# Optimization experiments

Measured on AMD Instinct MI355X. Metric: run time of the kernel, lower is better.

The kernel has to match this reference:

```python
import jax, jax.numpy as jnp
import numpy as np

D_MODEL = 1024
B, S = 4, 2048


def setup_inputs() -> dict:
    key = jax.random.key(0)
    kx, km, kq, kk, kv, ko = jax.random.split(key, 6)
    x = jax.random.normal(kx, (B, S, D_MODEL), dtype=jnp.float32)
    mask = jax.random.randint(km, (B, S, S), 0, 2).astype(jnp.bool_)
    # flax Dense default kernel init: lecun_normal-ish; plain scaled normal is fine for a reference
    init_scale = 1.0 / np.sqrt(D_MODEL)
    Wq = jax.random.normal(kq, (D_MODEL, D_MODEL), dtype=jnp.float32) * init_scale
    Wk = jax.random.normal(kk, (D_MODEL, D_MODEL), dtype=jnp.float32) * init_scale
    Wv = jax.random.normal(kv, (D_MODEL, D_MODEL), dtype=jnp.float32) * init_scale
    Wo = jax.random.normal(ko, (D_MODEL, D_MODEL), dtype=jnp.float32) * init_scale
    return {"x": x, "mask": mask, "Wq": Wq, "Wk": Wk, "Wv": Wv, "Wo": Wo}


def reference(x, mask, Wq, Wk, Wv, Wo):
    # QKV projections (use_bias=False)
    q = jnp.einsum('bsd,de->bse', x, Wq)
    k = jnp.einsum('bsd,de->bse', x, Wk)
    v = jnp.einsum('bsd,de->bse', x, Wv)
    scale = jnp.sqrt(jnp.asarray(q.shape[-1], x.dtype)).astype(x.dtype)
    # [B, S, S] attention scores
    attn_scores = jnp.einsum('bqd,bkd->bqk', q, k) / scale
    attn_scores = jnp.where(mask, attn_scores, jnp.asarray(-1e10, x.dtype))
    attn_weights = jax.nn.softmax(attn_scores, axis=-1)
    attn_output = jnp.einsum('bqk,bkd->bqd', attn_weights, v)
    return jnp.einsum('bsd,de->bse', attn_output, Wo)
```

## Files before the change

kernel.cpp:

```cpp
#include <hip/hip_runtime.h>


#define DM 1024
#define SQ 2048
#define NB 4
typedef unsigned short U16;
typedef short bhalf8 __attribute__((ext_vector_type(8)));
typedef float f32x4 __attribute__((ext_vector_type(4)));

__device__ inline U16 f2bf(float f) {
  unsigned int u = __float_as_uint(f);
  u += 0x7FFFu + ((u >> 16) & 1u);
  return (U16)(u >> 16);
}
__device__ inline float2 bfp2(unsigned int u) {
  float2 r;
  r.x = __uint_as_float(u << 16);
  r.y = __uint_as_float(u & 0xffff0000u);
  return r;
}
__device__ inline unsigned int packbf(float a, float b) {
  return (unsigned int)f2bf(a) | ((unsigned int)f2bf(b) << 16);
}

__global__ __launch_bounds__(256) void conv_f32_bf16(
    const float* __restrict__ src, U16* __restrict__ dst, float* __restrict__ rs) {
  int idx = blockIdx.x * 256 + threadIdx.x;
  if (idx < NB * SQ) rs[idx] = 0.f;
  int i = idx * 8;
  float4 a = *(const float4*)(src + i);
  float4 b = *(const float4*)(src + i + 4);
  uint4 w;
  w.x = packbf(a.x, a.y); w.y = packbf(a.z, a.w);
  w.z = packbf(b.x, b.y); w.w = packbf(b.z, b.w);
  *(uint4*)(dst + i) = w;
}

__device__ inline void ldcvt16(const float* p, U16* d) {
#pragma unroll
  for (int i = 0; i < 4; ++i) {
    float4 f = *(const float4*)(p + i * 4);
    d[i * 4 + 0] = f2bf(f.x); d[i * 4 + 1] = f2bf(f.y);
    d[i * 4 + 2] = f2bf(f.z); d[i * 4 + 3] = f2bf(f.w);
  }
}
__device__ inline void ldcvt16(const U16* p, U16* d) {
  uint4 a = *(const uint4*)p;
  uint4 b = *(const uint4*)(p + 8);
  *(uint4*)d = a;
  *(uint4*)(d + 8) = b;
}

__global__ __launch_bounds__(256) void transp_w4(
    const float* __restrict__ Wq, const float* __restrict__ Wk,
    const float* __restrict__ Wo, const float* __restrict__ Wv,
    U16* __restrict__ WT, U16* __restrict__ WoT, U16* __restrict__ Wv16) {
  __shared__ U16 tile[64][72];
  const int z = blockIdx.z;
  const int r0 = blockIdx.y * 64, c0 = blockIdx.x * 64;
  const int t = threadIdx.x;
  const int tr = t >> 2, tc = (t & 3) * 16;
  if (z == 3) {
    U16 vals[16];
    ldcvt16(Wv + (size_t)(r0 + tr) * DM + c0 + tc, vals);
    U16* op = Wv16 + (size_t)(r0 + tr) * DM + c0 + tc;
    *(uint4*)op = *(uint4*)&vals[0];
    *(uint4*)(op + 8) = *(uint4*)&vals[8];
    return;
  }
  const float* src = (z == 0) ? Wq : (z == 1) ? Wk : Wo;
  U16* d = (z == 2) ? WoT : WT + (size_t)z * DM * DM;
  ldcvt16(src + (size_t)(r0 + tr) * DM + c0 + tc, &tile[tr][tc]);
  __syncthreads();
  U16 vals[16];
#pragma unroll
  for (int m = 0; m < 16; ++m) vals[m] = tile[tc + m][tr];
  U16* op = d + (size_t)(c0 + tr) * DM + r0 + tc;
  *(uint4*)op = *(uint4*)&vals[0];
  *(uint4*)(op + 8) = *(uint4*)&vals[8];
}

__global__ __launch_bounds__(256) void transp_bf16(
    const U16* __restrict__ src, U16* __restrict__ dst, int R, int C) {
  __shared__ U16 tile[64][72];
  const int z = blockIdx.z;
  src += (size_t)z * R * C;
  dst += (size_t)z * R * C;
  const int r0 = blockIdx.y * 64, c0 = blockIdx.x * 64;
  const int t = threadIdx.x;
  const int tr = t >> 2, tc = (t & 3) * 16;
  ldcvt16(src + (size_t)(r0 + tr) * C + c0 + tc, &tile[tr][tc]);
  __syncthreads();
  U16 vals[16];
#pragma unroll
  for (int m = 0; m < 16; ++m) vals[m] = tile[tc + m][tr];
  U16* op = dst + (size_t)(c0 + tr) * R + r0 + tc;
  *(uint4*)op = *(uint4*)&vals[0];
  *(uint4*)(op + 8) = *(uint4*)&vals[8];
}

template <int EP>
__global__ __launch_bounds__(256) void gemm_mfma(
    const U16* __restrict__ A, const U16* __restrict__ B, void* __restrict__ Cv,
    int M, int N, int K, long long sA, long long sB, long long sC,
    const int* __restrict__ mask, float* __restrict__ rowsum, float scale) {
  __shared__ U16 As[128 * 72];
  __shared__ U16 Bs[128 * 72];
  const int t = threadIdx.x;
  const int lane = t & 63, wave = t >> 6;
  const int wm = wave >> 1, wn = wave & 1;
  const int q = lane >> 4, ln = lane & 15;
  const int z = blockIdx.z;
  const int m0 = blockIdx.y * 128, n0 = blockIdx.x * 128;
  A += (size_t)z * sA;
  B += (size_t)z * sB;

  f32x4 acc[4][4] = {};

  const int srow = t >> 3;
  const int scol = (t & 7) * 8;

  for (int k0 = 0; k0 < K; k0 += 64) {
    const U16* ga = A + (size_t)(m0 + srow) * K + k0 + scol;
    const U16* gb = B + (size_t)(n0 + srow) * K + k0 + scol;
#pragma unroll
    for (int it = 0; it < 4; ++it) {
      uint4 va = *(const uint4*)(ga + (size_t)it * 32 * K);
      uint4 vb = *(const uint4*)(gb + (size_t)it * 32 * K);
      *(uint4*)&As[(it * 32 + srow) * 72 + scol] = va;
      *(uint4*)&Bs[(it * 32 + srow) * 72 + scol] = vb;
    }
    __syncthreads();
#pragma unroll
    for (int kk = 0; kk < 64; kk += 32) {
      bhalf8 af[4], bg[4];
#pragma unroll
      for (int i = 0; i < 4; ++i) {
        af[i] = *(const bhalf8*)&As[(wm * 64 + i * 16 + ln) * 72 + kk + q * 8];
        bg[i] = *(const bhalf8*)&Bs[(wn * 64 + i * 16 + ln) * 72 + kk + q * 8];
      }
#pragma unroll
      for (int i = 0; i < 4; ++i)
#pragma unroll
        for (int j = 0; j < 4; ++j)
          acc[i][j] = __builtin_amdgcn_mfma_f32_16x16x32_bf16(af[i], bg[j], acc[i][j], 0, 0, 0);
    }
    __syncthreads();
  }

#pragma unroll
  for (int i = 0; i < 4; ++i) {
#pragma unroll
    for (int r = 0; r < 4; ++r) {
      const int rr = m0 + wm * 64 + i * 16 + q * 4 + r;
      float linv = 0.f;
      if constexpr (EP == 2) linv = 1.0f / (rowsum[(size_t)z * M + rr] + 1e-30f);
      float psum = 0.f;
#pragma unroll
      for (int j = 0; j < 4; ++j) {
        const int c = n0 + wn * 64 + j * 16 + ln;
        float v = acc[i][j][r];
        if constexpr (EP == 0) {
          ((U16*)Cv)[(size_t)z * sC + (size_t)rr * N + c] = f2bf(v);
        } else if constexpr (EP == 1) {
          int mk = mask[((size_t)z * M + rr) * N + c];
          float p = mk ? __expf(v * scale) : 0.f;
          U16 pb = f2bf(p);
          ((U16*)Cv)[(size_t)z * sC + (size_t)rr * N + c] = pb;
          psum += __uint_as_float((unsigned int)pb << 16);
        } else {
          ((float*)Cv)[(size_t)z * sC + (size_t)rr * N + c] = v * linv;
        }
      }
      if constexpr (EP == 1) {
#pragma unroll
        for (int off = 8; off > 0; off >>= 1) psum += __shfl_xor(psum, off, 64);
        if (ln == 0) atomicAdd(&rowsum[(size_t)z * M + rr], psum);
      }
    }
  }
}

__device__ inline float4 load4(const float* p) { return *(const float4*)p; }
__device__ inline float4 load4(const U16* p) {
  uint2 w = *(const uint2*)p;
  float2 f0 = bfp2(w.x), f1 = bfp2(w.y);
  return make_float4(f0.x, f0.y, f1.x, f1.y);
}
__device__ inline void store4(float* p, float a, float b, float c, float d) {
  *(float4*)p = make_float4(a, b, c, d);
}
__device__ inline void store4(U16* p, float a, float b, float c, float d) {
  uint2 w;
  w.x = packbf(a, b);
  w.y = packbf(c, d);
  *(uint2*)p = w;
}
template <typename TA, typename TB, typename TC>
__global__ __launch_bounds__(256) void gemm_t(
    const TA* __restrict__ A, const TB* __restrict__ B,
    TC* __restrict__ C, int M, int N, int K) {
  __shared__ float As[16][64];
  __shared__ float Bs[16][64];
  const int t = threadIdx.x;
  const int tx = t & 15, ty = t >> 4;
  const int m0 = blockIdx.y * 64;
  const int n0 = blockIdx.x * 64;
  const int arow = t >> 2, akq = (t & 3) * 4;
  const int brow = t >> 4, bcg = (t & 15) * 4;
  float acc[4][4] = {};
  for (int k0 = 0; k0 < K; k0 += 16) {
    {
      float4 f = load4(A + (size_t)(m0 + arow) * K + k0 + akq);
      As[akq + 0][arow] = f.x; As[akq + 1][arow] = f.y;
      As[akq + 2][arow] = f.z; As[akq + 3][arow] = f.w;
    }
    {
      float4 f = load4(B + (size_t)(k0 + brow) * N + n0 + bcg);
      *(float4*)&Bs[brow][bcg] = f;
    }
    __syncthreads();
#pragma unroll
    for (int kk = 0; kk < 16; ++kk) {
      float4 a = *(const float4*)&As[kk][ty * 4];
      float4 b = *(const float4*)&Bs[kk][tx * 4];
      float av[4] = {a.x, a.y, a.z, a.w};
      float bv[4] = {b.x, b.y, b.z, b.w};
#pragma unroll
      for (int i = 0; i < 4; ++i)
#pragma unroll
        for (int j = 0; j < 4; ++j) acc[i][j] += av[i] * bv[j];
    }
    __syncthreads();
  }
#pragma unroll
  for (int i = 0; i < 4; ++i)
    store4(&C[(size_t)(m0 + ty * 4 + i) * N + n0 + tx * 4],
           acc[i][0], acc[i][1], acc[i][2], acc[i][3]);
}
__global__ __launch_bounds__(256) void flash_wave(
    const U16* __restrict__ Q, const U16* __restrict__ Kd,
    const U16* __restrict__ V, const int* __restrict__ mask,
    U16* __restrict__ O) {
  __shared__ float q_s[4][DM];
  const int t = threadIdx.x;
  const int w = t >> 6;
  const int lane = t & 63;
  const int row = blockIdx.x * 4 + w;
  const int b = row >> 11;
  const size_t bo = (size_t)b * SQ * DM;
  const size_t mrow0 = (size_t)row * SQ;
  {
    const U16* qp = Q + (size_t)row * DM + lane * 16;
    uint4 w0 = *(const uint4*)qp;
    uint4 w1 = *(const uint4*)(qp + 8);
    float* dst = &q_s[w][lane * 16];
    float2 f;
    f = bfp2(w0.x); dst[0] = f.x;  dst[1] = f.y;
    f = bfp2(w0.y); dst[2] = f.x;  dst[3] = f.y;
    f = bfp2(w0.z); dst[4] = f.x;  dst[5] = f.y;
    f = bfp2(w0.w); dst[6] = f.x;  dst[7] = f.y;
    f = bfp2(w1.x); dst[8] = f.x;  dst[9] = f.y;
    f = bfp2(w1.y); dst[10] = f.x; dst[11] = f.y;
    f = bfp2(w1.z); dst[12] = f.x; dst[13] = f.y;
    f = bfp2(w1.w); dst[14] = f.x; dst[15] = f.y;
  }
  __syncthreads();
  float m = -3.0e38f, l = 0.f;
  float o[16] = {};
  const int dbase = lane * 16;
  const float* qrow = q_s[w];
  for (int j0 = 0; j0 < SQ; j0 += 64) {
    float s;
    {
      const U16* kp = Kd + bo + (size_t)(j0 + lane) * DM;
      float acc = 0.f;
      for (int d = 0; d < DM; d += 8) {
        uint4 kw = *(const uint4*)(kp + d);
        float2 a0 = bfp2(kw.x), a1 = bfp2(kw.y), a2 = bfp2(kw.z), a3 = bfp2(kw.w);
        acc += qrow[d] * a0.x + qrow[d + 1] * a0.y + qrow[d + 2] * a1.x +
               qrow[d + 3] * a1.y + qrow[d + 4] * a2.x + qrow[d + 5] * a2.y +
               qrow[d + 6] * a3.x + qrow[d + 7] * a3.y;
      }
      s = acc * 0.03125f;
      if (mask[mrow0 + j0 + lane] == 0) s = -1e10f;
    }
    float ms = s;
#pragma unroll
    for (int off = 32; off > 0; off >>= 1) ms = fmaxf(ms, __shfl_xor(ms, off, 64));
    float mn = fmaxf(m, ms);
    float alpha = __expf(m - mn);
    float p = __expf(s - mn);
    float ps = p;
#pragma unroll
    for (int off = 32; off > 0; off >>= 1) ps += __shfl_xor(ps, off, 64);
    l = l * alpha + ps;
    m = mn;
#pragma unroll
    for (int k = 0; k < 16; ++k) o[k] *= alpha;
    const U16* vp = V + bo + (size_t)j0 * DM + dbase;
    for (int j = 0; j < 64; ++j) {
      float pj = __shfl(p, j, 64);
      uint4 v0 = *(const uint4*)(vp + (size_t)j * DM);
      uint4 v1 = *(const uint4*)(vp + (size_t)j * DM + 8);
      float2 f0 = bfp2(v0.x), f1 = bfp2(v0.y), f2 = bfp2(v0.z), f3 = bfp2(v0.w);
      float2 g0 = bfp2(v1.x), g1 = bfp2(v1.y), g2 = bfp2(v1.z), g3 = bfp2(v1.w);
      o[0] += pj * f0.x;  o[1] += pj * f0.y;  o[2] += pj * f1.x;  o[3] += pj * f1.y;
      o[4] += pj * f2.x;  o[5] += pj * f2.y;  o[6] += pj * f3.x;  o[7] += pj * f3.y;
      o[8] += pj * g0.x;  o[9] += pj * g0.y;  o[10] += pj * g1.x; o[11] += pj * g1.y;
      o[12] += pj * g2.x; o[13] += pj * g2.y; o[14] += pj * g3.x; o[15] += pj * g3.y;
    }
  }
  float linv = (l > 0.f) ? (1.0f / l) : 0.f;
  U16* op = O + (size_t)row * DM + dbase;
  uint4 r0, r1;
  r0.x = packbf(o[0] * linv, o[1] * linv);
  r0.y = packbf(o[2] * linv, o[3] * linv);
  r0.z = packbf(o[4] * linv, o[5] * linv);
  r0.w = packbf(o[6] * linv, o[7] * linv);
  r1.x = packbf(o[8] * linv, o[9] * linv);
  r1.y = packbf(o[10] * linv, o[11] * linv);
  r1.z = packbf(o[12] * linv, o[13] * linv);
  r1.w = packbf(o[14] * linv, o[15] * linv);
  *(uint4*)op = r0;
  *(uint4*)(op + 8) = r1;
}

extern "C" void kernel_launch(void* const* d_in, const int* in_sizes, int n_in,
                              void* d_out, int out_size, void* d_ws, size_t ws_size,
                              hipStream_t stream) {
  const float* x  = (const float*)d_in[0];
  const int* mask = (const int*)d_in[1];
  const float* Wq = (const float*)d_in[2];
  const float* Wk = (const float*)d_in[3];
  const float* Wv = (const float*)d_in[4];
  const float* Wo = (const float*)d_in[5];
  float* out = (float*)d_out;

  const size_t MB = 1u << 20;
  const size_t E = (size_t)NB * SQ * DM;
  const size_t WE = (size_t)DM * DM;

  if (ws_size >= 121 * MB) {
    char* ws = (char*)d_ws;
    U16* WT   = (U16*)ws;
    U16* WoT  = (U16*)(ws + 6 * MB);
    U16* x16  = (U16*)(ws + 8 * MB);
    U16* Q16  = (U16*)(ws + 24 * MB);
    U16* K16  = (U16*)(ws + 40 * MB);
    U16* U16b = (U16*)(ws + 56 * MB);
    U16* Wv16 = (U16*)(ws + 72 * MB);
    U16* UT16 = (U16*)(ws + 72 * MB);
    U16* P16  = (U16*)(ws + 88 * MB);
    float* rs = (float*)(ws + 120 * MB);

    conv_f32_bf16<<<dim3(E / (256 * 8)), 256, 0, stream>>>(x, x16, rs);
    transp_w4<<<dim3(16, 16, 4), 256, 0, stream>>>(Wq, Wk, Wo, Wv, WT, WoT, Wv16);

    gemm_mfma<0><<<dim3(DM / 128, DM / 128, 1), 256, 0, stream>>>(
        WoT, Wv16, WT + 2 * WE, DM, DM, DM, 0, 0, 0, nullptr, nullptr, 0.f);

    gemm_mfma<0><<<dim3(DM / 128, (NB * SQ) / 128, 3), 256, 0, stream>>>(
        x16, WT, Q16, NB * SQ, DM, DM,
        0, (long long)WE, (long long)E, nullptr, nullptr, 0.f);

    transp_bf16<<<dim3(DM / 64, SQ / 64, NB), 256, 0, stream>>>(U16b, UT16, SQ, DM);

    gemm_mfma<1><<<dim3(SQ / 128, SQ / 128, NB), 256, 0, stream>>>(
        Q16, K16, P16, SQ, SQ, DM,
        (long long)SQ * DM, (long long)SQ * DM, (long long)SQ * SQ,
        mask, rs, 0.03125f);

    gemm_mfma<2><<<dim3(DM / 128, SQ / 128, NB), 256, 0, stream>>>(
        P16, UT16, out, SQ, DM, SQ,
        (long long)SQ * SQ, (long long)DM * SQ, (long long)SQ * DM,
        nullptr, rs, 0.f);
  } else {
    U16* Kw = (U16*)d_ws;
    U16* Vw = Kw + E;
    U16* Qw = Vw + E;
    U16* Ow = Qw;
    dim3 blk(256);
    dim3 gg(DM / 64, (NB * SQ) / 64);
    gemm_t<float, float, U16><<<gg, blk, 0, stream>>>(x, Wk, Kw, NB * SQ, DM, DM);
    gemm_t<float, float, U16><<<gg, blk, 0, stream>>>(x, Wv, Vw, NB * SQ, DM, DM);
    gemm_t<float, float, U16><<<gg, blk, 0, stream>>>(x, Wq, Qw, NB * SQ, DM, DM);
    flash_wave<<<dim3((NB * SQ) / 4), blk, 0, stream>>>(Qw, Kw, Vw, mask, Ow);
    gemm_t<U16, float, float><<<gg, blk, 0, stream>>>(Ow, Wo, out, NB * SQ, DM, DM);
  }
}
```

Measured before the change: 358.2 us.

## Add double-buffered direct-to-LDS GEMM with larger tiles for main matmuls

Introduces a new 512-thread GEMM kernel that loads A/B tiles straight into LDS with global_load_lds_dwordx4 and double-buffers them, so the next tile's load overlaps the current tile's MFMA work. Block tiles grow to 256x128 or 256x256, which raises data reuse per block. The QKV projection, the masked-score GEMM and the PV GEMM all switch to it. In exchange, LDS use is larger and occupancy lower, and the unpadded 64-wide LDS rows may cause bank conflicts on the fragment reads. The grid for the score GEMM also shrinks, which can hurt load balance.

After: 348.1 us. 1.03x faster.

```diff
diff --git a/kernel.cpp b/kernel.cpp
--- a/kernel.cpp
+++ b/kernel.cpp
@@ -21,6 +21,16 @@
 }
 __device__ inline unsigned int packbf(float a, float b) {
   return (unsigned int)f2bf(a) | ((unsigned int)f2bf(b) << 16);
+}
+
+__device__ __forceinline__ void gload16(const U16* g, const U16* l) {
+  unsigned int m0v =
+      (unsigned int)__builtin_amdgcn_readfirstlane((int)(unsigned long long)l);
+  asm volatile("s_mov_b32 m0, %0\n\t"
+               "global_load_lds_dwordx4 %1, off"
+               :
+               : "s"(m0v), "v"(g)
+               : "memory");
 }
 
 __global__ __launch_bounds__(256) void conv_f32_bf16(
@@ -153,6 +163,112 @@
 #pragma unroll
     for (int r = 0; r < 4; ++r) {
       const int rr = m0 + wm * 64 + i * 16 + q * 4 + r;
+      float linv = 0.f;
+      if constexpr (EP == 2) linv = 1.0f / (rowsum[(size_t)z * M + rr] + 1e-30f);
+      float psum = 0.f;
+#pragma unroll
+      for (int j = 0; j < 4; ++j) {
+        const int c = n0 + wn * 64 + j * 16 + ln;
+        float v = acc[i][j][r];
+        if constexpr (EP == 0) {
+          ((U16*)Cv)[(size_t)z * sC + (size_t)rr * N + c] = f2bf(v);
+        } else if constexpr (EP == 1) {
+          int mk = mask[((size_t)z * M + rr) * N + c];
+          float p = mk ? __expf(v * scale) : 0.f;
+          U16 pb = f2bf(p);
+          ((U16*)Cv)[(size_t)z * sC + (size_t)rr * N + c] = pb;
+          psum += __uint_as_float((unsigned int)pb << 16);
+        } else {
+          ((float*)Cv)[(size_t)z * sC + (size_t)rr * N + c] = v * linv;
+        }
+      }
+      if constexpr (EP == 1) {
+#pragma unroll
+        for (int off = 8; off > 0; off >>= 1) psum += __shfl_xor(psum, off, 64);
+        if (ln == 0) atomicAdd(&rowsum[(size_t)z * M + rr], psum);
+      }
+    }
+  }
+}
+
+template <int EP, int FM>
+__global__ __launch_bounds__(512) void gemm2(
+    const U16* __restrict__ A, const U16* __restrict__ B, void* __restrict__ Cv,
+    int M, int N, int K, long long sA, long long sB, long long sC,
+    const int* __restrict__ mask, float* __restrict__ rowsum, float scale) {
+  constexpr int WN = (FM == 4) ? 2 : 4;
+  constexpr int BN = WN * 64;
+  __shared__ __attribute__((aligned(16))) U16 As[2][256 * 64];
+  __shared__ __attribute__((aligned(16))) U16 Bs[2][BN * 64];
+  const int t = threadIdx.x;
+  const int lane = t & 63, wave = t >> 6;
+  const int wm = wave / WN, wn = wave % WN;
+  const int q = lane >> 4, ln = lane & 15;
+  const int z = blockIdx.z;
+  const int m0 = blockIdx.y * 256, n0 = blockIdx.x * BN;
+  const U16* Ab = A + (size_t)z * sA + (size_t)m0 * K;
+  const U16* Bb = B + (size_t)z * sB + (size_t)n0 * K;
+  const U16* gA = Ab + (size_t)(wave * 8 + (lane >> 3)) * K + (lane & 7) * 8;
+  const U16* gB = Bb + (size_t)(wave * 8 + (lane >> 3)) * K + (lane & 7) * 8;
+  const U16* lA = &As[0][wave * 8 * 64];
+  const U16* lB = &Bs[0][wave * 8 * 64];
+
+  f32x4 acc[FM][4] = {};
+  const int NT = K >> 6;
+
+#define STAGE2(bufi, koff)                                                   \
+  {                                                                          \
+    _Pragma("unroll") for (int c = 0; c < 4; ++c)                            \
+        gload16(gA + (size_t)(c * 64) * K + (koff),                          \
+                lA + (bufi) * (256 * 64) + c * (64 * 64));                   \
+    _Pragma("unroll") for (int c = 0; c < BN / 64; ++c)                      \
+        gload16(gB + (size_t)(c * 64) * K + (koff),                          \
+                lB + (bufi) * (BN * 64) + c * (64 * 64));                    \
+  }
+
+#define COMPUTE2(bufi)                                                       \
+  {                                                                          \
+    _Pragma("unroll") for (int kk = 0; kk < 64; kk += 32) {                  \
+      bhalf8 af[FM], bg[4];                                                  \
+      _Pragma("unroll") for (int i = 0; i < FM; ++i)                         \
+          af[i] = *(const bhalf8*)&As[bufi][(wm * (FM * 16) + i * 16 + ln) * 64 + kk + q * 8]; \
+      _Pragma("unroll") for (int j = 0; j < 4; ++j)                          \
+          bg[j] = *(const bhalf8*)&Bs[bufi][(wn * 64 + j * 16 + ln) * 64 + kk + q * 8]; \
+      _Pragma("unroll") for (int i = 0; i < FM; ++i)                         \
+          _Pragma("unroll") for (int j = 0; j < 4; ++j)                      \
+              acc[i][j] = __builtin_amdgcn_mfma_f32_16x16x32_bf16(af[i], bg[j], acc[i][j], 0, 0, 0); \
+    }                                                                        \
+  }
+
+#define VMBAR                                            \
+  {                                                      \
+    asm volatile("s_waitcnt vmcnt(0)" ::: "memory");     \
+    __syncthreads();                                     \
+  }
+
+  STAGE2(0, 0);
+  VMBAR;
+  for (int tk = 2; tk < NT; tk += 2) {
+    STAGE2(1, (tk - 1) * 64);
+    COMPUTE2(0);
+    VMBAR;
+    STAGE2(0, tk * 64);
+    COMPUTE2(1);
+    VMBAR;
+  }
+  STAGE2(1, (NT - 1) * 64);
+  COMPUTE2(0);
+  VMBAR;
+  COMPUTE2(1);
+#undef STAGE2
+#undef COMPUTE2
+#undef VMBAR
+
+#pragma unroll
+  for (int i = 0; i < FM; ++i) {
+#pragma unroll
+    for (int r = 0; r < 4; ++r) {
+      const int rr = m0 + wm * (FM * 16) + i * 16 + q * 4 + r;
       float linv = 0.f;
       if constexpr (EP == 2) linv = 1.0f / (rowsum[(size_t)z * M + rr] + 1e-30f);
       float psum = 0.f;
@@ -360,18 +476,18 @@
     gemm_mfma<0><<<dim3(DM / 128, DM / 128, 1), 256, 0, stream>>>(
         WoT, Wv16, WT + 2 * WE, DM, DM, DM, 0, 0, 0, nullptr, nullptr, 0.f);
 
-    gemm_mfma<0><<<dim3(DM / 128, (NB * SQ) / 128, 3), 256, 0, stream>>>(
+    gemm2<0, 4><<<dim3(DM / 128, (NB * SQ) / 256, 3), 512, 0, stream>>>(
         x16, WT, Q16, NB * SQ, DM, DM,
         0, (long long)WE, (long long)E, nullptr, nullptr, 0.f);
 
     transp_bf16<<<dim3(DM / 64, SQ / 64, NB), 256, 0, stream>>>(U16b, UT16, SQ, DM);
 
-    gemm_mfma<1><<<dim3(SQ / 128, SQ / 128, NB), 256, 0, stream>>>(
+    gemm2<1, 8><<<dim3(SQ / 256, SQ / 256, NB), 512, 0, stream>>>(
         Q16, K16, P16, SQ, SQ, DM,
         (long long)SQ * DM, (long long)SQ * DM, (long long)SQ * SQ,
         mask, rs, 0.03125f);
 
-    gemm_mfma<2><<<dim3(DM / 128, SQ / 128, NB), 256, 0, stream>>>(
+    gemm2<2, 4><<<dim3(DM / 128, SQ / 256, NB), 512, 0, stream>>>(
         P16, UT16, out, SQ, DM, SQ,
         (long long)SQ * SQ, (long long)DM * SQ, (long long)SQ * DM,
         nullptr, rs, 0.f);
```
